# Optimization experiments

Hardware: AMD Instinct MI355X
Metric: run time of the kernel (lower is better)

Reference implementation:

```python
import jax, jax.numpy as jnp
import numpy as np

N, E, HN, K = 4096, 8192, 1024, 8
NF, EF = 128, 64
NH = [256, 256]
EH = [64, 64]
EMB = NH[-1] + len(EH)  # 258
BN_EPS = 1e-5


def setup_inputs() -> dict:
    key = jax.random.key(0)
    ks = jax.random.split(key, 16)

    def nrm(k, shape, fan):
        return jax.random.normal(k, shape, jnp.float32) / np.float32(np.sqrt(fan))

    return {
        "X_n": jax.random.normal(ks[0], (N, NF), jnp.float32),
        "X_e": jax.random.normal(ks[1], (E, EF), jnp.float32),
        # row-normalized-ish adjacency and scaled Laplacian to keep activations bounded
        "A_tilde": jax.random.uniform(ks[2], (N, N), jnp.float32) / np.float32(N),
        "L1_tilde": jax.random.normal(ks[3], (E, E), jnp.float32) / np.float32(np.sqrt(E)),
        "B1": jax.random.normal(ks[4], (N, E), jnp.float32) / np.float32(np.sqrt(E)),
        # GNN params (Linear stores weight as [out, in])
        "gnn_W1": nrm(ks[5], (NH[0], NF), NF), "gnn_b1": jnp.zeros((NH[0],), jnp.float32),
        "gnn_W2": nrm(ks[6], (NH[1], NH[0]), NH[0]), "gnn_b2": jnp.zeros((NH[1],), jnp.float32),
        # HoSC layer 1: in=EF, out=EH[0]
        "hosc_W1": nrm(ks[7], (EH[0], EF), EF), "hosc_b1": jnp.zeros((EH[0],), jnp.float32),
        "bn1_g": jnp.ones((EH[0],), jnp.float32), "bn1_b": jnp.zeros((EH[0],), jnp.float32),
        # HoSC layer 2: in=1 (after channel-max), out=EH[1]
        "hosc_W2": nrm(ks[8], (EH[1], 1), 1), "hosc_b2": jnp.zeros((EH[1],), jnp.float32),
        "bn2_g": jnp.ones((EH[1],), jnp.float32), "bn2_b": jnp.zeros((EH[1],), jnp.float32),
        # heads
        "node_W": nrm(ks[9], (1, EMB), EMB), "node_b": jnp.zeros((1,), jnp.float32),
        "edge_W": nrm(ks[10], (1, len(EH)), len(EH)), "edge_b": jnp.zeros((1,), jnp.float32),
        "hyper_W": nrm(ks[11], (1, EMB), EMB), "hyper_b": jnp.zeros((1,), jnp.float32),
        "hyperedges": jax.random.randint(ks[12], (HN, K), 0, N, jnp.int64),
    }


def _bn(x, g, b):
    # training-mode BatchNorm1d: biased batch statistics over rows
    m = jnp.mean(x, axis=0)
    v = jnp.var(x, axis=0)
    return g * (x - m) / jnp.sqrt(v + BN_EPS) + b


def _hosc_layer(Z, L1, W, bias, g, b):
    Zt = Z @ W.T + bias            # [E, out]
    Zc = L1 @ Zt                   # [E, out]
    Zp = jax.nn.relu(_bn(Zc, g, b))
    return jnp.max(Zp, axis=1, keepdims=True)  # [E, 1]


def reference(X_n, X_e, A_tilde, L1_tilde, B1,
              gnn_W1, gnn_b1, gnn_W2, gnn_b2,
              hosc_W1, hosc_b1, bn1_g, bn1_b,
              hosc_W2, hosc_b2, bn2_g, bn2_b,
              node_W, node_b, edge_W, edge_b, hyper_W, hyper_b,
              hyperedges):
    # --- GNN over nodes ---
    H = jax.nn.relu((A_tilde @ X_n) @ gnn_W1.T + gnn_b1)   # [N, 256]
    H_n = jax.nn.relu((A_tilde @ H) @ gnn_W2.T + gnn_b2)   # [N, 256]

    # --- HoSC over edges ---
    Z1 = _hosc_layer(X_e, L1_tilde, hosc_W1, hosc_b1, bn1_g, bn1_b)  # [E, 1]
    Z2 = _hosc_layer(Z1, L1_tilde, hosc_W2, hosc_b2, bn2_g, bn2_b)   # [E, 1]
    Z_H = jnp.concatenate([Z1, Z2], axis=1)                 # [E, 2]

    # --- fuse edge info into nodes ---
    H_e = B1 @ Z_H                                          # [N, 2]
    Hcat = jnp.concatenate([H_n, H_e], axis=1)              # [N, 258]

    node_prob = jax.nn.sigmoid(Hcat @ node_W.T + node_b).squeeze(-1)  # [N]
    edge_prob = jax.nn.sigmoid(Z_H @ edge_W.T + edge_b).squeeze(-1)   # [E]

    # vectorized hyperedge gather-mean-linear-sigmoid (fixed-size hyperedges)
    hfeat = Hcat[hyperedges].mean(axis=1)                   # [HN, 258]
    hyperedge_prob = jax.nn.sigmoid(hfeat @ hyper_W.T + hyper_b)  # [HN, 1]

    return node_prob, edge_prob, hyperedge_prob, Hcat
```

## Files before the change

kernel.cpp:

```cpp
#include <hip/hip_runtime.h>
#include <hip/hip_bf16.h>

using f32x4  = __attribute__((ext_vector_type(4))) float;
using u32x4  = __attribute__((ext_vector_type(4))) unsigned int;
using bf16x8 = __attribute__((ext_vector_type(8))) short;

__device__ __forceinline__ ushort f2bf(float x) {
    union { __hip_bfloat16 h; ushort u; } cv;
    cv.h = __float2bfloat16(x);
    return cv.u;
}
__device__ __forceinline__ unsigned pk2(float lo, float hi) {
    return (unsigned)f2bf(lo) | ((unsigned)f2bf(hi) << 16);
}
__device__ __forceinline__ float sigmoidf_(float x) { return 1.f / (1.f + expf(-x)); }

template<int NSUM, bool A_BF16, bool ABR, bool SPLIT, bool RELU, bool BF16_OUT, bool HAS_BIAS>
__device__ __forceinline__ void gemm_body(
    ushort* As, ushort* Bs,
    const void* __restrict__ Avoid, const ushort* __restrict__ B,
    const float* __restrict__ abias, const float* __restrict__ bias,
    float* __restrict__ Cf, ushort* __restrict__ Cb,
    int M, int N, int K, int ldc, int kPerChunk, long pStride,
    int bx, int by, int bz)
{
    const int tid  = threadIdx.x;
    const int lane = tid & 63;
    const int wid  = tid >> 6;
    const int wr   = wid >> 1, wc = wid & 1;
    const int g    = lane >> 4, lr = lane & 15;
    const long m0  = (long)bx * 128;
    const int  n0  = by * 64;

    int kbeg = 0, kend = K;
    if (SPLIT) { kbeg = bz * kPerChunk; kend = kbeg + kPerChunk; if (kend > K) kend = K; }

    const int bkr = tid & 31;
    const int bcb = tid >> 5;

    const float*  Af = (const float*)Avoid;
    const ushort* Ab = (const ushort*)Avoid;

    f32x4 pa[4];
    u32x4 pab[2];
    u32x4 pb;

    auto loadT = [&](int k0) {
        if (A_BF16) {
#pragma unroll
            for (int i = 0; i < 2; i++) {
                int s = tid + 256 * i; int row = s >> 2, c8 = s & 3;
                pab[i] = *(const u32x4*)(Ab + (m0 + row) * (long)K + k0 + c8 * 8);
            }
        } else {
#pragma unroll
            for (int i = 0; i < 4; i++) {
                int s = tid + 256 * i; int row = s >> 3, c4 = s & 7;
                const float* base = Af + (m0 + row) * (long)K + k0 + c4 * 4;
                f32x4 v = *(const f32x4*)base;
                if (NSUM > 0) {
#pragma unroll
                    for (int z = 1; z < NSUM; z++) v += *(const f32x4*)(base + z * pStride);
                }
                if (ABR) {
                    f32x4 bq = *(const f32x4*)(abias + k0 + c4 * 4);
                    v.x = fmaxf(v.x + bq.x, 0.f);
                    v.y = fmaxf(v.y + bq.y, 0.f);
                    v.z = fmaxf(v.z + bq.z, 0.f);
                    v.w = fmaxf(v.w + bq.w, 0.f);
                }
                pa[i] = v;
            }
        }
        pb = *(const u32x4*)(B + (long)(k0 + bkr) * N + n0 + bcb * 8);
    };
    auto storeT = [&]() {
        if (A_BF16) {
#pragma unroll
            for (int i = 0; i < 2; i++) {
                int s = tid + 256 * i; int row = s >> 2, c8 = s & 3;
                *(u32x4*)(&As[row * 40 + c8 * 8]) = pab[i];
            }
        } else {
#pragma unroll
            for (int i = 0; i < 4; i++) {
                int s = tid + 256 * i; int row = s >> 3, c4 = s & 7;
                ushort4 w;
                w.x = f2bf(pa[i].x); w.y = f2bf(pa[i].y);
                w.z = f2bf(pa[i].z); w.w = f2bf(pa[i].w);
                *(ushort4*)(&As[row * 40 + c4 * 4]) = w;
            }
        }
        const ushort* p8 = (const ushort*)&pb;
#pragma unroll
        for (int j = 0; j < 8; j++) Bs[(bcb * 8 + j) * 40 + bkr] = p8[j];
    };

    f32x4 acc[4][2] = {};

    const int nk = (kend - kbeg) >> 5;
    loadT(kbeg);
    for (int t = 0; t < nk; ++t) {
        storeT();
        __syncthreads();
        if (t + 1 < nk) loadT(kbeg + ((t + 1) << 5));
        bf16x8 af[4], bfr[2];
#pragma unroll
        for (int fm = 0; fm < 4; fm++)
            af[fm] = *(const bf16x8*)(&As[(wr * 64 + fm * 16 + lr) * 40 + g * 8]);
#pragma unroll
        for (int fn = 0; fn < 2; fn++)
            bfr[fn] = *(const bf16x8*)(&Bs[(wc * 32 + fn * 16 + lr) * 40 + g * 8]);
#pragma unroll
        for (int fm = 0; fm < 4; fm++)
#pragma unroll
            for (int fn = 0; fn < 2; fn++)
                acc[fm][fn] = __builtin_amdgcn_mfma_f32_16x16x32_bf16(af[fm], bfr[fn], acc[fm][fn], 0, 0, 0);
        __syncthreads();
    }

    if (SPLIT) {
        float* P = Cf + (long)bz * M * N;
#pragma unroll
        for (int fm = 0; fm < 4; fm++)
#pragma unroll
            for (int fn = 0; fn < 2; fn++)
#pragma unroll
                for (int rr = 0; rr < 4; rr++) {
                    long row = m0 + wr * 64 + fm * 16 + g * 4 + rr;
                    int  col = n0 + wc * 32 + fn * 16 + lr;
                    P[row * N + col] = acc[fm][fn][rr];
                }
    } else {
#pragma unroll
        for (int fm = 0; fm < 4; fm++)
#pragma unroll
            for (int fn = 0; fn < 2; fn++)
#pragma unroll
                for (int rr = 0; rr < 4; rr++) {
                    long row = m0 + wr * 64 + fm * 16 + g * 4 + rr;
                    int  col = n0 + wc * 32 + fn * 16 + lr;
                    float v = acc[fm][fn][rr];
                    if (HAS_BIAS) v += bias[col];
                    if (RELU) v = fmaxf(v, 0.f);
                    if (BF16_OUT) Cb[row * ldc + col] = f2bf(v);
                    else          Cf[row * ldc + col] = v;
                }
    }
}

__global__ __launch_bounds__(256)
void prep_k(const float* __restrict__ A, ushort* __restrict__ Abf,
            const float* __restrict__ Xn, const float* __restrict__ W1, ushort* __restrict__ T1,
            const float* __restrict__ Xe, const float* __restrict__ Wh,
            const float* __restrict__ hb, ushort* __restrict__ Zt1,
            const float* __restrict__ W2, ushort* __restrict__ W2t,
            float* __restrict__ stats)
{
    __shared__ float xs[1024];
    int b = blockIdx.x, t = threadIdx.x;
    if (b < 8192) {
        long j = (long)b * 256 + t;
        f32x4 v0 = ((const f32x4*)A)[2 * j];
        f32x4 v1 = ((const f32x4*)A)[2 * j + 1];
        u32x4 w;
        w.x = pk2(v0.x, v0.y); w.y = pk2(v0.z, v0.w);
        w.z = pk2(v1.x, v1.y); w.w = pk2(v1.z, v1.w);
        ((u32x4*)Abf)[j] = w;
    } else if (b < 8704) {
        int r0 = (b - 8192) * 8;
        for (int idx = t; idx < 1024; idx += 256) xs[idx] = Xn[(long)r0 * 128 + idx];
        __syncthreads();
        float acc[8] = {};
        const float* wrow = W1 + (long)t * 128;
        for (int i = 0; i < 128; i++) {
            float w = wrow[i];
#pragma unroll
            for (int r = 0; r < 8; r++) acc[r] += xs[r * 128 + i] * w;
        }
#pragma unroll
        for (int r = 0; r < 8; r++) T1[(long)(r0 + r) * 256 + t] = f2bf(acc[r]);
    } else if (b < 10752) {
        int row = (b - 8704) * 4 + (t >> 6);
        int o   = t & 63;
        const float* xr = Xe + (long)row * 64;
        const float* wr = Wh + (long)o * 64;
        float acc = hb[o];
#pragma unroll 8
        for (int i = 0; i < 64; i++) acc += xr[i] * wr[i];
        Zt1[(long)row * 64 + o] = f2bf(acc);
    } else if (b < 11008) {
        int j = (b - 10752) * 256 + t;
        int i = j >> 8, o = j & 255;
        W2t[j] = f2bf(W2[o * 256 + i]);
    } else {
        if (t < 256) stats[t] = 0.f;
    }
}

__device__ __forceinline__ void bnred_body(int b, const float* __restrict__ P,
                                           float* __restrict__ Zc,
                                           float* __restrict__ gsum, float* __restrict__ gsq)
{
    const long MN = 8192 * 64;
    int t = threadIdx.x;
    int c = t & 63, rg = t >> 6;
    float sx = 0.f, sq = 0.f;
    int base = b * 32 + rg;
#pragma unroll 4
    for (int i = 0; i < 8; i++) {
        long idx = (long)(base + 4 * i) * 64 + c;
        float x = 0.f;
#pragma unroll
        for (int z = 0; z < 8; z++) x += P[idx + z * MN];
        Zc[idx] = x;
        sx += x; sq += x * x;
    }
    __shared__ float ls[256], lq[256];
    ls[t] = sx; lq[t] = sq;
    __syncthreads();
    if (t < 64) {
        float a = ls[t] + ls[t + 64] + ls[t + 128] + ls[t + 192];
        float q = lq[t] + lq[t + 64] + lq[t + 128] + lq[t + 192];
        atomicAdd(&gsum[t], a);
        atomicAdd(&gsq[t], q);
    }
}

__device__ __forceinline__ void z1_body(int b, const float* __restrict__ Zc,
                                        const float* __restrict__ gsum, const float* __restrict__ gsq,
                                        const float* __restrict__ g, const float* __restrict__ bb,
                                        float* __restrict__ Z1)
{
    int w = threadIdx.x >> 6, lane = threadIdx.x & 63;
    int row = b * 4 + w;
    const float inv = 1.f / 8192.f;
    float m = gsum[lane] * inv;
    float v = gsq[lane] * inv - m * m;
    float x = Zc[row * 64 + lane];
    float y = fmaxf(g[lane] * (x - m) * rsqrtf(v + 1e-5f) + bb[lane], 0.f);
#pragma unroll
    for (int o = 32; o > 0; o >>= 1) y = fmaxf(y, __shfl_xor(y, o));
    if (lane == 0) Z1[row] = y;
}

__device__ __forceinline__ void pass2_body(int row, const float* __restrict__ L1,
                                           const float* __restrict__ Z1,
                                           float* __restrict__ s, float* __restrict__ r)
{
    int t = threadIdx.x;
    int l = t & 63, w = t >> 6;
    const f32x4* rp = (const f32x4*)(L1 + (long)row * 8192);
    const f32x4* z4 = (const f32x4*)Z1;
    float as = 0.f, ar = 0.f;
#pragma unroll 4
    for (int k = 0; k < 8; k++) {
        f32x4 v = rp[t + 256 * k];
        f32x4 z = z4[t + 256 * k];
        as += v.x * z.x + v.y * z.y + v.z * z.z + v.w * z.w;
        ar += v.x + v.y + v.z + v.w;
    }
#pragma unroll
    for (int o = 32; o > 0; o >>= 1) { as += __shfl_xor(as, o); ar += __shfl_xor(ar, o); }
    __shared__ float sw[4], rw[4];
    if (l == 0) { sw[w] = as; rw[w] = ar; }
    __syncthreads();
    if (t == 0) {
        s[row] = sw[0] + sw[1] + sw[2] + sw[3];
        r[row] = rw[0] + rw[1] + rw[2] + rw[3];
    }
    __syncthreads();
}

__device__ __forceinline__ void hcatred_body(int b, const float* __restrict__ P,
                                             const float* __restrict__ b2, float* __restrict__ hcat)
{
    const long MNq = (long)4096 * 256 / 4;
    int j = b * 256 + threadIdx.x;
    int row = j >> 6, c4 = (j & 63) * 4;
    const f32x4* Q = (const f32x4*)P;
    f32x4 v = Q[j] + Q[j + MNq] + Q[j + 2 * MNq] + Q[j + 3 * MNq];
    f32x4 bq = *(const f32x4*)(b2 + c4);
    float* dst = hcat + (long)row * 258 + c4;
    float2 lo = { fmaxf(v.x + bq.x, 0.f), fmaxf(v.y + bq.y, 0.f) };
    float2 hi = { fmaxf(v.z + bq.z, 0.f), fmaxf(v.w + bq.w, 0.f) };
    *(float2*)dst = lo;
    *(float2*)(dst + 2) = hi;
}

__global__ __launch_bounds__(256)
void dual_a_k(const float* __restrict__ L1, const ushort* __restrict__ Zt1, float* __restrict__ Pa,
              const ushort* __restrict__ Abf, const ushort* __restrict__ T1, float* __restrict__ Pb)
{
    __shared__ ushort As[128 * 40];
    __shared__ ushort Bs[64 * 40];
    int bid = blockIdx.x;
    if (bid < 512) {
        gemm_body<0, false, false, true, false, false, false>(
            As, Bs, L1, Zt1, nullptr, nullptr, Pa, nullptr,
            8192, 64, 8192, 64, 1024, 0, bid & 63, 0, bid >> 6);
    } else {
        int b = bid - 512;
        gemm_body<0, true, false, true, false, false, false>(
            As, Bs, Abf, T1, nullptr, nullptr, Pb, nullptr,
            4096, 256, 4096, 256, 1024, 0, b & 31, (b >> 5) & 3, b >> 7);
    }
}

__global__ __launch_bounds__(256)
void dual_b_k(const float* __restrict__ Pb, const float* __restrict__ gb1,
              const ushort* __restrict__ W2t, ushort* __restrict__ T2,
              const float* __restrict__ Pa, float* __restrict__ Zc1,
              float* __restrict__ gsum, float* __restrict__ gsq)
{
    __shared__ ushort As[128 * 40];
    __shared__ ushort Bs[64 * 40];
    int bid = blockIdx.x;
    if (bid < 128) {
        gemm_body<4, false, true, false, false, true, false>(
            As, Bs, Pb, W2t, gb1, nullptr, nullptr, T2,
            4096, 256, 256, 256, 0, (long)4096 * 256, bid & 31, bid >> 5, 0);
    } else {
        bnred_body(bid - 128, Pa, Zc1, gsum, gsq);
    }
}

__global__ __launch_bounds__(256)
void dual_c_k(const ushort* __restrict__ Abf, const ushort* __restrict__ T2, float* __restrict__ Pa,
              const float* __restrict__ Zc1, const float* __restrict__ gsum,
              const float* __restrict__ gsq, const float* __restrict__ bn1g,
              const float* __restrict__ bn1b, float* __restrict__ Z1)
{
    __shared__ ushort As[128 * 40];
    __shared__ ushort Bs[64 * 40];
    int bid = blockIdx.x;
    if (bid < 512) {
        gemm_body<0, true, false, true, false, false, false>(
            As, Bs, Abf, T2, nullptr, nullptr, Pa, nullptr,
            4096, 256, 4096, 256, 1024, 0, bid & 31, (bid >> 5) & 3, bid >> 7);
    } else {
        z1_body(bid - 512, Zc1, gsum, gsq, bn1g, bn1b, Z1);
    }
}

__global__ __launch_bounds__(256)
void dual_d_k(const float* __restrict__ Pa, const float* __restrict__ gb2, float* __restrict__ hcat,
              const float* __restrict__ L1, const float* __restrict__ Z1,
              float* __restrict__ s, float* __restrict__ r)
{
    int bid = blockIdx.x;
    if (bid < 1024) {
        hcatred_body(bid, Pa, gb2, hcat);
    } else {
        int pb = bid - 1024;
#pragma unroll
        for (int i = 0; i < 4; i++)
            pass2_body(i * 2048 + pb, L1, Z1, s, r);
    }
}

__global__ __launch_bounds__(256)
void z2_edge_k(const float* __restrict__ s, const float* __restrict__ r,
               const float* __restrict__ W2, const float* __restrict__ b2,
               const float* __restrict__ g2, const float* __restrict__ bb2,
               const float* __restrict__ eW, const float* __restrict__ eb,
               const float* __restrict__ Z1,
               float* __restrict__ Z2, float* __restrict__ edge_out)
{
    int t = threadIdx.x, l = t & 63, w = t >> 6;
    float Ss = 0, Sr = 0, Sss = 0, Srr = 0, Ssr = 0;
    for (int i = t; i < 8192; i += 256) {
        float sv = s[i], rv = r[i];
        Ss += sv; Sr += rv; Sss += sv * sv; Srr += rv * rv; Ssr += sv * rv;
    }
#pragma unroll
    for (int o = 32; o > 0; o >>= 1) {
        Ss += __shfl_xor(Ss, o); Sr += __shfl_xor(Sr, o);
        Sss += __shfl_xor(Sss, o); Srr += __shfl_xor(Srr, o); Ssr += __shfl_xor(Ssr, o);
    }
    __shared__ float buf[4][5];
    if (l == 0) { buf[w][0] = Ss; buf[w][1] = Sr; buf[w][2] = Sss; buf[w][3] = Srr; buf[w][4] = Ssr; }
    __syncthreads();
    float S0 = buf[0][0] + buf[1][0] + buf[2][0] + buf[3][0];
    float S1 = buf[0][1] + buf[1][1] + buf[2][1] + buf[3][1];
    float S2 = buf[0][2] + buf[1][2] + buf[2][2] + buf[3][2];
    float S3 = buf[0][3] + buf[1][3] + buf[2][3] + buf[3][3];
    float S4 = buf[0][4] + buf[1][4] + buf[2][4] + buf[3][4];

    int row = blockIdx.x * 4 + w;
    const float inv = 1.f / 8192.f;
    float ms = S0 * inv, mr = S1 * inv;
    float vs = S2 * inv - ms * ms;
    float vr = S3 * inv - mr * mr;
    float cv = S4 * inv - ms * mr;
    float w2 = W2[l], bz = b2[l];
    float mc = w2 * ms + bz * mr;
    float vc = w2 * w2 * vs + 2.f * w2 * bz * cv + bz * bz * vr;
    float x  = w2 * s[row] + bz * r[row];
    float y  = fmaxf(g2[l] * (x - mc) * rsqrtf(vc + 1e-5f) + bb2[l], 0.f);
#pragma unroll
    for (int o = 32; o > 0; o >>= 1) y = fmaxf(y, __shfl_xor(y, o));
    if (l == 0) {
        Z2[row] = y;
        float e = Z1[row] * eW[0] + y * eW[1] + eb[0];
        edge_out[row] = sigmoidf_(e);
    }
}

__global__ __launch_bounds__(256) void he_node_k(const float* __restrict__ B1, const float* __restrict__ Z1,
                                                 const float* __restrict__ Z2, float* __restrict__ hcat,
                                                 const float* __restrict__ nW, const float* __restrict__ nb,
                                                 float* __restrict__ node_out)
{
    int t = threadIdx.x;
    int l = t & 63, w = t >> 6;
    __shared__ float s1[4], s2[4], s3[4];
    const f32x4* z1v = (const f32x4*)Z1;
    const f32x4* z2v = (const f32x4*)Z2;
#pragma unroll
    for (int i = 0; i < 4; i++) {
        int n = i * 1024 + blockIdx.x;
        const f32x4* rp = (const f32x4*)(B1 + (long)n * 8192);
        float a1 = 0.f, a2 = 0.f;
#pragma unroll 4
        for (int k = 0; k < 8; k++) {
            f32x4 v = rp[t + 256 * k];
            f32x4 p = z1v[t + 256 * k];
            f32x4 q = z2v[t + 256 * k];
            a1 += v.x * p.x + v.y * p.y + v.z * p.z + v.w * p.w;
            a2 += v.x * q.x + v.y * q.y + v.z * q.z + v.w * q.w;
        }
        float d = hcat[(long)n * 258 + t] * nW[t];
#pragma unroll
        for (int o = 32; o > 0; o >>= 1) {
            a1 += __shfl_xor(a1, o); a2 += __shfl_xor(a2, o); d += __shfl_xor(d, o);
        }
        if (l == 0) { s1[w] = a1; s2[w] = a2; s3[w] = d; }
        __syncthreads();
        if (t == 0) {
            float A1 = s1[0] + s1[1] + s1[2] + s1[3];
            float A2 = s2[0] + s2[1] + s2[2] + s2[3];
            float D  = s3[0] + s3[1] + s3[2] + s3[3];
            hcat[(long)n * 258 + 256] = A1;
            hcat[(long)n * 258 + 257] = A2;
            node_out[n] = sigmoidf_(D + A1 * nW[256] + A2 * nW[257] + nb[0]);
        }
        __syncthreads();
    }
}

__global__ __launch_bounds__(256) void hyper_k(const void* __restrict__ he_idx,
                                               const float* __restrict__ hcat,
                                               const float* __restrict__ hW, const float* __restrict__ hb,
                                               float* __restrict__ out)
{
    int w = threadIdx.x >> 6, lane = threadIdx.x & 63;
    int h = blockIdx.x * 4 + w;
    const unsigned int* u = (const unsigned int*)he_idx;
    unsigned int odd = u[2 * lane + 1];
    bool is64 = __all(odd == 0u);
    float acc = 0.f;
    for (int k = 0; k < 8; k++) {
        int idx;
        if (is64) idx = (int)((const long long*)he_idx)[h * 8 + k];
        else      idx = ((const int*)he_idx)[h * 8 + k];
        const float* hr = hcat + (long)idx * 258;
        for (int d = lane; d < 258; d += 64) acc += hr[d] * hW[d];
    }
    acc *= 0.125f;
#pragma unroll
    for (int o = 32; o > 0; o >>= 1) acc += __shfl_xor(acc, o);
    if (lane == 0) out[h] = sigmoidf_(acc + hb[0]);
}

extern "C" void kernel_launch(void* const* d_in, const int* in_sizes, int n_in,
                              void* d_out, int out_size, void* d_ws, size_t ws_size,
                              hipStream_t stream)
{
    const float* X_n  = (const float*)d_in[0];
    const float* X_e  = (const float*)d_in[1];
    const float* A_t  = (const float*)d_in[2];
    const float* L1   = (const float*)d_in[3];
    const float* B1   = (const float*)d_in[4];
    const float* gW1  = (const float*)d_in[5];
    const float* gb1  = (const float*)d_in[6];
    const float* gW2  = (const float*)d_in[7];
    const float* gb2  = (const float*)d_in[8];
    const float* hW1  = (const float*)d_in[9];
    const float* hb1  = (const float*)d_in[10];
    const float* bn1g = (const float*)d_in[11];
    const float* bn1b = (const float*)d_in[12];
    const float* hW2  = (const float*)d_in[13];
    const float* hb2  = (const float*)d_in[14];
    const float* bn2g = (const float*)d_in[15];
    const float* bn2b = (const float*)d_in[16];
    const float* nW   = (const float*)d_in[17];
    const float* nb   = (const float*)d_in[18];
    const float* eW   = (const float*)d_in[19];
    const float* ebb  = (const float*)d_in[20];
    const float* yW   = (const float*)d_in[21];
    const float* yb   = (const float*)d_in[22];
    const void*  he   = d_in[23];

    float* out       = (float*)d_out;
    float* out_node  = out;
    float* out_edge  = out + 4096;
    float* out_hyper = out + 12288;
    float* hcat      = out + 13312;

    size_t off = 0;
    auto alloc = [&](size_t bytes) {
        void* p = (char*)d_ws + off;
        off = (off + bytes + 255) & ~(size_t)255;
        return p;
    };
    ushort* Abf    = (ushort*)alloc((size_t)4096 * 4096 * 2);
    ushort* T1     = (ushort*)alloc(4096 * 256 * 2);
    ushort* T2     = (ushort*)alloc(4096 * 256 * 2);
    ushort* Zt1    = (ushort*)alloc(8192 * 64 * 2);
    ushort* W2t    = (ushort*)alloc(256 * 256 * 2);
    float*  Zc1    = (float*)alloc(8192 * 64 * 4);
    float*  stats  = (float*)alloc(256 * 4);
    float*  gsum   = stats;
    float*  gsq    = stats + 64;
    float*  Z1     = (float*)alloc(8192 * 4);
    float*  Z2     = (float*)alloc(8192 * 4);
    float*  sbuf   = (float*)alloc(8192 * 4);
    float*  rbuf   = (float*)alloc(8192 * 4);
    float*  Pa     = (float*)alloc((size_t)8192 * 64 * 8 * 4);
    float*  Pb     = (float*)alloc((size_t)4096 * 256 * 4 * 4);

    prep_k<<<11009, 256, 0, stream>>>(A_t, Abf, X_n, gW1, T1, X_e, hW1, hb1, Zt1,
                                      gW2, W2t, stats);

    dual_a_k<<<1024, 256, 0, stream>>>(L1, Zt1, Pa, Abf, T1, Pb);

    dual_b_k<<<384, 256, 0, stream>>>(Pb, gb1, W2t, T2, Pa, Zc1, gsum, gsq);

    dual_c_k<<<2560, 256, 0, stream>>>(Abf, T2, Pa, Zc1, gsum, gsq, bn1g, bn1b, Z1);

    dual_d_k<<<3072, 256, 0, stream>>>(Pa, gb2, hcat, L1, Z1, sbuf, rbuf);

    z2_edge_k<<<2048, 256, 0, stream>>>(sbuf, rbuf, hW2, hb2, bn2g, bn2b,
                                        eW, ebb, Z1, Z2, out_edge);

    he_node_k<<<1024, 256, 0, stream>>>(B1, Z1, Z2, hcat, nW, nb, out_node);

    hyper_k<<<256, 256, 0, stream>>>(he, hcat, yW, yb, out_hyper);
}
```

Baseline: 301.7 us.

## Merge all stage kernels into one persistent cooperative kernel with grid syncs

Replaces the eight separate kernel launches with one cooperative persistent kernel. Each former kernel becomes a grid-stride phase separated by __threadfence and grid.sync, and the grid is sized from the occupancy query (capped at 2048 blocks). The aim is to remove per-launch overhead and inter-kernel gaps. In exchange, the phases are limited to a fixed resident grid, grid-wide barriers are added, and the launch-bounds occupancy hint may constrain registers in the GEMM phases.

```diff
diff --git a/kernel.cpp b/kernel.cpp
--- a/kernel.cpp
+++ b/kernel.cpp
@@ -1,5 +1,8 @@
 #include <hip/hip_runtime.h>
 #include <hip/hip_bf16.h>
+#include <hip/hip_cooperative_groups.h>
+
+namespace cg = cooperative_groups;
 
 using f32x4  = __attribute__((ext_vector_type(4))) float;
 using u32x4  = __attribute__((ext_vector_type(4))) unsigned int;
@@ -149,278 +152,235 @@
     }
 }
 
-__global__ __launch_bounds__(256)
-void prep_k(const float* __restrict__ A, ushort* __restrict__ Abf,
-            const float* __restrict__ Xn, const float* __restrict__ W1, ushort* __restrict__ T1,
-            const float* __restrict__ Xe, const float* __restrict__ Wh,
-            const float* __restrict__ hb, ushort* __restrict__ Zt1,
-            const float* __restrict__ W2, ushort* __restrict__ W2t,
-            float* __restrict__ stats)
+struct MegaArgs {
+    const float *A, *Xn, *W1, *Xe, *Wh, *hb1, *W2;
+    ushort *Abf, *T1, *Zt1, *W2t, *T2;
+    const float *L1, *B1;
+    float *stats;
+    float *Zc1, *Z1, *Z2, *sbuf, *rbuf, *Pa, *Pb;
+    const float *gb1, *gb2, *bn1g, *bn1b, *hW2, *hb2, *bn2g, *bn2b;
+    const float *nW, *nb, *eW, *eb, *yW, *yb;
+    const void  *he;
+    float *hcat, *out_node, *out_edge, *out_hyper;
+};
+
+__global__ __launch_bounds__(256, 4) void mega_k(MegaArgs a)
 {
-    __shared__ float xs[1024];
-    int b = blockIdx.x, t = threadIdx.x;
-    if (b < 8192) {
-        long j = (long)b * 256 + t;
-        f32x4 v0 = ((const f32x4*)A)[2 * j];
-        f32x4 v1 = ((const f32x4*)A)[2 * j + 1];
-        u32x4 w;
-        w.x = pk2(v0.x, v0.y); w.y = pk2(v0.z, v0.w);
-        w.z = pk2(v1.x, v1.y); w.w = pk2(v1.z, v1.w);
-        ((u32x4*)Abf)[j] = w;
-    } else if (b < 8704) {
-        int r0 = (b - 8192) * 8;
-        for (int idx = t; idx < 1024; idx += 256) xs[idx] = Xn[(long)r0 * 128 + idx];
-        __syncthreads();
-        float acc[8] = {};
-        const float* wrow = W1 + (long)t * 128;
-        for (int i = 0; i < 128; i++) {
-            float w = wrow[i];
-#pragma unroll
-            for (int r = 0; r < 8; r++) acc[r] += xs[r * 128 + i] * w;
-        }
-#pragma unroll
-        for (int r = 0; r < 8; r++) T1[(long)(r0 + r) * 256 + t] = f2bf(acc[r]);
-    } else if (b < 10752) {
-        int row = (b - 8704) * 4 + (t >> 6);
-        int o   = t & 63;
-        const float* xr = Xe + (long)row * 64;
-        const float* wr = Wh + (long)o * 64;
-        float acc = hb[o];
-#pragma unroll 8
-        for (int i = 0; i < 64; i++) acc += xr[i] * wr[i];
-        Zt1[(long)row * 64 + o] = f2bf(acc);
-    } else if (b < 11008) {
-        int j = (b - 10752) * 256 + t;
-        int i = j >> 8, o = j & 255;
-        W2t[j] = f2bf(W2[o * 256 + i]);
-    } else {
-        if (t < 256) stats[t] = 0.f;
-    }
-}
-
-__device__ __forceinline__ void bnred_body(int b, const float* __restrict__ P,
-                                           float* __restrict__ Zc,
-                                           float* __restrict__ gsum, float* __restrict__ gsq)
-{
-    const long MN = 8192 * 64;
-    int t = threadIdx.x;
-    int c = t & 63, rg = t >> 6;
-    float sx = 0.f, sq = 0.f;
-    int base = b * 32 + rg;
-#pragma unroll 4
-    for (int i = 0; i < 8; i++) {
-        long idx = (long)(base + 4 * i) * 64 + c;
-        float x = 0.f;
-#pragma unroll
-        for (int z = 0; z < 8; z++) x += P[idx + z * MN];
-        Zc[idx] = x;
-        sx += x; sq += x * x;
-    }
-    __shared__ float ls[256], lq[256];
-    ls[t] = sx; lq[t] = sq;
-    __syncthreads();
-    if (t < 64) {
-        float a = ls[t] + ls[t + 64] + ls[t + 128] + ls[t + 192];
-        float q = lq[t] + lq[t + 64] + lq[t + 128] + lq[t + 192];
-        atomicAdd(&gsum[t], a);
-        atomicAdd(&gsq[t], q);
-    }
-}
-
-__device__ __forceinline__ void z1_body(int b, const float* __restrict__ Zc,
-                                        const float* __restrict__ gsum, const float* __restrict__ gsq,
-                                        const float* __restrict__ g, const float* __restrict__ bb,
-                                        float* __restrict__ Z1)
-{
-    int w = threadIdx.x >> 6, lane = threadIdx.x & 63;
-    int row = b * 4 + w;
-    const float inv = 1.f / 8192.f;
-    float m = gsum[lane] * inv;
-    float v = gsq[lane] * inv - m * m;
-    float x = Zc[row * 64 + lane];
-    float y = fmaxf(g[lane] * (x - m) * rsqrtf(v + 1e-5f) + bb[lane], 0.f);
-#pragma unroll
-    for (int o = 32; o > 0; o >>= 1) y = fmaxf(y, __shfl_xor(y, o));
-    if (lane == 0) Z1[row] = y;
-}
-
-__device__ __forceinline__ void pass2_body(int row, const float* __restrict__ L1,
-                                           const float* __restrict__ Z1,
-                                           float* __restrict__ s, float* __restrict__ r)
-{
-    int t = threadIdx.x;
-    int l = t & 63, w = t >> 6;
-    const f32x4* rp = (const f32x4*)(L1 + (long)row * 8192);
-    const f32x4* z4 = (const f32x4*)Z1;
-    float as = 0.f, ar = 0.f;
-#pragma unroll 4
-    for (int k = 0; k < 8; k++) {
-        f32x4 v = rp[t + 256 * k];
-        f32x4 z = z4[t + 256 * k];
-        as += v.x * z.x + v.y * z.y + v.z * z.z + v.w * z.w;
-        ar += v.x + v.y + v.z + v.w;
-    }
-#pragma unroll
-    for (int o = 32; o > 0; o >>= 1) { as += __shfl_xor(as, o); ar += __shfl_xor(ar, o); }
-    __shared__ float sw[4], rw[4];
-    if (l == 0) { sw[w] = as; rw[w] = ar; }
-    __syncthreads();
-    if (t == 0) {
-        s[row] = sw[0] + sw[1] + sw[2] + sw[3];
-        r[row] = rw[0] + rw[1] + rw[2] + rw[3];
-    }
-    __syncthreads();
-}
-
-__device__ __forceinline__ void hcatred_body(int b, const float* __restrict__ P,
-                                             const float* __restrict__ b2, float* __restrict__ hcat)
-{
-    const long MNq = (long)4096 * 256 / 4;
-    int j = b * 256 + threadIdx.x;
-    int row = j >> 6, c4 = (j & 63) * 4;
-    const f32x4* Q = (const f32x4*)P;
-    f32x4 v = Q[j] + Q[j + MNq] + Q[j + 2 * MNq] + Q[j + 3 * MNq];
-    f32x4 bq = *(const f32x4*)(b2 + c4);
-    float* dst = hcat + (long)row * 258 + c4;
-    float2 lo = { fmaxf(v.x + bq.x, 0.f), fmaxf(v.y + bq.y, 0.f) };
-    float2 hi = { fmaxf(v.z + bq.z, 0.f), fmaxf(v.w + bq.w, 0.f) };
-    *(float2*)dst = lo;
-    *(float2*)(dst + 2) = hi;
-}
-
-__global__ __launch_bounds__(256)
-void dual_a_k(const float* __restrict__ L1, const ushort* __restrict__ Zt1, float* __restrict__ Pa,
-              const ushort* __restrict__ Abf, const ushort* __restrict__ T1, float* __restrict__ Pb)
-{
+    cg::grid_group grid = cg::this_grid();
     __shared__ ushort As[128 * 40];
     __shared__ ushort Bs[64 * 40];
-    int bid = blockIdx.x;
-    if (bid < 512) {
-        gemm_body<0, false, false, true, false, false, false>(
-            As, Bs, L1, Zt1, nullptr, nullptr, Pa, nullptr,
-            8192, 64, 8192, 64, 1024, 0, bid & 63, 0, bid >> 6);
-    } else {
-        int b = bid - 512;
-        gemm_body<0, true, false, true, false, false, false>(
-            As, Bs, Abf, T1, nullptr, nullptr, Pb, nullptr,
-            4096, 256, 4096, 256, 1024, 0, b & 31, (b >> 5) & 3, b >> 7);
-    }
-}
-
-__global__ __launch_bounds__(256)
-void dual_b_k(const float* __restrict__ Pb, const float* __restrict__ gb1,
-              const ushort* __restrict__ W2t, ushort* __restrict__ T2,
-              const float* __restrict__ Pa, float* __restrict__ Zc1,
-              float* __restrict__ gsum, float* __restrict__ gsq)
-{
-    __shared__ ushort As[128 * 40];
-    __shared__ ushort Bs[64 * 40];
-    int bid = blockIdx.x;
-    if (bid < 128) {
-        gemm_body<4, false, true, false, false, true, false>(
-            As, Bs, Pb, W2t, gb1, nullptr, nullptr, T2,
-            4096, 256, 256, 256, 0, (long)4096 * 256, bid & 31, bid >> 5, 0);
-    } else {
-        bnred_body(bid - 128, Pa, Zc1, gsum, gsq);
-    }
-}
-
-__global__ __launch_bounds__(256)
-void dual_c_k(const ushort* __restrict__ Abf, const ushort* __restrict__ T2, float* __restrict__ Pa,
-              const float* __restrict__ Zc1, const float* __restrict__ gsum,
-              const float* __restrict__ gsq, const float* __restrict__ bn1g,
-              const float* __restrict__ bn1b, float* __restrict__ Z1)
-{
-    __shared__ ushort As[128 * 40];
-    __shared__ ushort Bs[64 * 40];
-    int bid = blockIdx.x;
-    if (bid < 512) {
-        gemm_body<0, true, false, true, false, false, false>(
-            As, Bs, Abf, T2, nullptr, nullptr, Pa, nullptr,
-            4096, 256, 4096, 256, 1024, 0, bid & 31, (bid >> 5) & 3, bid >> 7);
-    } else {
-        z1_body(bid - 512, Zc1, gsum, gsq, bn1g, bn1b, Z1);
-    }
-}
-
-__global__ __launch_bounds__(256)
-void dual_d_k(const float* __restrict__ Pa, const float* __restrict__ gb2, float* __restrict__ hcat,
-              const float* __restrict__ L1, const float* __restrict__ Z1,
-              float* __restrict__ s, float* __restrict__ r)
-{
-    int bid = blockIdx.x;
-    if (bid < 1024) {
-        hcatred_body(bid, Pa, gb2, hcat);
-    } else {
-        int pb = bid - 1024;
-#pragma unroll
-        for (int i = 0; i < 4; i++)
-            pass2_body(i * 2048 + pb, L1, Z1, s, r);
-    }
-}
-
-__global__ __launch_bounds__(256)
-void z2_edge_k(const float* __restrict__ s, const float* __restrict__ r,
-               const float* __restrict__ W2, const float* __restrict__ b2,
-               const float* __restrict__ g2, const float* __restrict__ bb2,
-               const float* __restrict__ eW, const float* __restrict__ eb,
-               const float* __restrict__ Z1,
-               float* __restrict__ Z2, float* __restrict__ edge_out)
-{
-    int t = threadIdx.x, l = t & 63, w = t >> 6;
-    float Ss = 0, Sr = 0, Sss = 0, Srr = 0, Ssr = 0;
-    for (int i = t; i < 8192; i += 256) {
-        float sv = s[i], rv = r[i];
-        Ss += sv; Sr += rv; Sss += sv * sv; Srr += rv * rv; Ssr += sv * rv;
-    }
-#pragma unroll
-    for (int o = 32; o > 0; o >>= 1) {
-        Ss += __shfl_xor(Ss, o); Sr += __shfl_xor(Sr, o);
-        Sss += __shfl_xor(Sss, o); Srr += __shfl_xor(Srr, o); Ssr += __shfl_xor(Ssr, o);
-    }
-    __shared__ float buf[4][5];
-    if (l == 0) { buf[w][0] = Ss; buf[w][1] = Sr; buf[w][2] = Sss; buf[w][3] = Srr; buf[w][4] = Ssr; }
-    __syncthreads();
-    float S0 = buf[0][0] + buf[1][0] + buf[2][0] + buf[3][0];
-    float S1 = buf[0][1] + buf[1][1] + buf[2][1] + buf[3][1];
-    float S2 = buf[0][2] + buf[1][2] + buf[2][2] + buf[3][2];
-    float S3 = buf[0][3] + buf[1][3] + buf[2][3] + buf[3][3];
-    float S4 = buf[0][4] + buf[1][4] + buf[2][4] + buf[3][4];
-
-    int row = blockIdx.x * 4 + w;
-    const float inv = 1.f / 8192.f;
-    float ms = S0 * inv, mr = S1 * inv;
-    float vs = S2 * inv - ms * ms;
-    float vr = S3 * inv - mr * mr;
-    float cv = S4 * inv - ms * mr;
-    float w2 = W2[l], bz = b2[l];
-    float mc = w2 * ms + bz * mr;
-    float vc = w2 * w2 * vs + 2.f * w2 * bz * cv + bz * bz * vr;
-    float x  = w2 * s[row] + bz * r[row];
-    float y  = fmaxf(g2[l] * (x - mc) * rsqrtf(vc + 1e-5f) + bb2[l], 0.f);
-#pragma unroll
-    for (int o = 32; o > 0; o >>= 1) y = fmaxf(y, __shfl_xor(y, o));
-    if (l == 0) {
-        Z2[row] = y;
-        float e = Z1[row] * eW[0] + y * eW[1] + eb[0];
-        edge_out[row] = sigmoidf_(e);
-    }
-}
-
-__global__ __launch_bounds__(256) void he_node_k(const float* __restrict__ B1, const float* __restrict__ Z1,
-                                                 const float* __restrict__ Z2, float* __restrict__ hcat,
-                                                 const float* __restrict__ nW, const float* __restrict__ nb,
-                                                 float* __restrict__ node_out)
-{
-    int t = threadIdx.x;
-    int l = t & 63, w = t >> 6;
-    __shared__ float s1[4], s2[4], s3[4];
-    const f32x4* z1v = (const f32x4*)Z1;
-    const f32x4* z2v = (const f32x4*)Z2;
-#pragma unroll
-    for (int i = 0; i < 4; i++) {
-        int n = i * 1024 + blockIdx.x;
-        const f32x4* rp = (const f32x4*)(B1 + (long)n * 8192);
+    const int G = gridDim.x;
+    const int t = threadIdx.x;
+    const int l = t & 63, w = t >> 6;
+
+    for (int u = blockIdx.x; u < 11009; u += G) {
+        if (u < 8192) {
+            long j = (long)u * 256 + t;
+            f32x4 v0 = ((const f32x4*)a.A)[2 * j];
+            f32x4 v1 = ((const f32x4*)a.A)[2 * j + 1];
+            u32x4 wv;
+            wv.x = pk2(v0.x, v0.y); wv.y = pk2(v0.z, v0.w);
+            wv.z = pk2(v1.x, v1.y); wv.w = pk2(v1.z, v1.w);
+            ((u32x4*)a.Abf)[j] = wv;
+        } else if (u < 8704) {
+            float* xs = (float*)As;
+            int r0 = (u - 8192) * 8;
+            __syncthreads();
+            for (int idx = t; idx < 1024; idx += 256) xs[idx] = a.Xn[(long)r0 * 128 + idx];
+            __syncthreads();
+            float acc[8] = {};
+            const float* wrow = a.W1 + (long)t * 128;
+            for (int i = 0; i < 128; i++) {
+                float wv = wrow[i];
+#pragma unroll
+                for (int r = 0; r < 8; r++) acc[r] += xs[r * 128 + i] * wv;
+            }
+#pragma unroll
+            for (int r = 0; r < 8; r++) a.T1[(long)(r0 + r) * 256 + t] = f2bf(acc[r]);
+        } else if (u < 10752) {
+            int row = (u - 8704) * 4 + w;
+            int o   = l;
+            const float* xr = a.Xe + (long)row * 64;
+            const float* wr = a.Wh + (long)o * 64;
+            float acc = a.hb1[o];
+#pragma unroll 8
+            for (int i = 0; i < 64; i++) acc += xr[i] * wr[i];
+            a.Zt1[(long)row * 64 + o] = f2bf(acc);
+        } else if (u < 11008) {
+            int j = (u - 10752) * 256 + t;
+            int i = j >> 8, o = j & 255;
+            a.W2t[j] = f2bf(a.W2[o * 256 + i]);
+        } else {
+            if (t < 128) a.stats[t] = 0.f;
+        }
+    }
+    __threadfence();
+    grid.sync();
+
+    for (int u = blockIdx.x; u < 1024; u += G) {
+        if (u < 512) {
+            gemm_body<0, false, false, true, false, false, false>(
+                As, Bs, a.L1, a.Zt1, nullptr, nullptr, a.Pa, nullptr,
+                8192, 64, 8192, 64, 1024, 0, u & 63, 0, u >> 6);
+        } else {
+            int b = u - 512;
+            gemm_body<0, true, false, true, false, false, false>(
+                As, Bs, a.Abf, a.T1, nullptr, nullptr, a.Pb, nullptr,
+                4096, 256, 4096, 256, 1024, 0, b & 31, (b >> 5) & 3, b >> 7);
+        }
+    }
+    __threadfence();
+    grid.sync();
+
+    for (int u = blockIdx.x; u < 384; u += G) {
+        if (u < 128) {
+            gemm_body<4, false, true, false, false, true, false>(
+                As, Bs, a.Pb, a.W2t, a.gb1, nullptr, nullptr, a.T2,
+                4096, 256, 256, 256, 0, (long)4096 * 256, u & 31, u >> 5, 0);
+        } else {
+            int b = u - 128;
+            const long MN = 8192 * 64;
+            int c = t & 63, rg = t >> 6;
+            float sx = 0.f, sq = 0.f;
+            int base = b * 32 + rg;
+#pragma unroll 4
+            for (int i = 0; i < 8; i++) {
+                long idx = (long)(base + 4 * i) * 64 + c;
+                float x = 0.f;
+#pragma unroll
+                for (int z = 0; z < 8; z++) x += a.Pa[idx + z * MN];
+                a.Zc1[idx] = x;
+                sx += x; sq += x * x;
+            }
+            float* ls = (float*)Bs;
+            float* lq = ls + 256;
+            __syncthreads();
+            ls[t] = sx; lq[t] = sq;
+            __syncthreads();
+            if (t < 64) {
+                float av = ls[t] + ls[t + 64] + ls[t + 128] + ls[t + 192];
+                float qv = lq[t] + lq[t + 64] + lq[t + 128] + lq[t + 192];
+                atomicAdd(&a.stats[t], av);
+                atomicAdd(&a.stats[64 + t], qv);
+            }
+            __syncthreads();
+        }
+    }
+    __threadfence();
+    grid.sync();
+
+    for (int u = blockIdx.x; u < 2560; u += G) {
+        if (u < 512) {
+            gemm_body<0, true, false, true, false, false, false>(
+                As, Bs, a.Abf, a.T2, nullptr, nullptr, a.Pa, nullptr,
+                4096, 256, 4096, 256, 1024, 0, u & 31, (u >> 5) & 3, u >> 7);
+        } else {
+            int b = u - 512;
+            int row = b * 4 + w;
+            const float inv = 1.f / 8192.f;
+            float m = a.stats[l] * inv;
+            float v = a.stats[64 + l] * inv - m * m;
+            float x = a.Zc1[row * 64 + l];
+            float y = fmaxf(a.bn1g[l] * (x - m) * rsqrtf(v + 1e-5f) + a.bn1b[l], 0.f);
+#pragma unroll
+            for (int o = 32; o > 0; o >>= 1) y = fmaxf(y, __shfl_xor(y, o));
+            if (l == 0) a.Z1[row] = y;
+        }
+    }
+    __threadfence();
+    grid.sync();
+
+    for (int u = blockIdx.x; u < 9216; u += G) {
+        if (u < 1024) {
+            const long MNq = (long)4096 * 256 / 4;
+            int j = u * 256 + t;
+            int row = j >> 6, c4 = (j & 63) * 4;
+            const f32x4* Q = (const f32x4*)a.Pa;
+            f32x4 v = Q[j] + Q[j + MNq] + Q[j + 2 * MNq] + Q[j + 3 * MNq];
+            f32x4 bq = *(const f32x4*)(a.gb2 + c4);
+            float* dst = a.hcat + (long)row * 258 + c4;
+            float2 lo = { fmaxf(v.x + bq.x, 0.f), fmaxf(v.y + bq.y, 0.f) };
+            float2 hi = { fmaxf(v.z + bq.z, 0.f), fmaxf(v.w + bq.w, 0.f) };
+            *(float2*)dst = lo;
+            *(float2*)(dst + 2) = hi;
+        } else {
+            int row = u - 1024;
+            const f32x4* rp = (const f32x4*)(a.L1 + (long)row * 8192);
+            const f32x4* z4 = (const f32x4*)a.Z1;
+            float as = 0.f, ar = 0.f;
+#pragma unroll 4
+            for (int k = 0; k < 8; k++) {
+                f32x4 v = rp[t + 256 * k];
+                f32x4 z = z4[t + 256 * k];
+                as += v.x * z.x + v.y * z.y + v.z * z.z + v.w * z.w;
+                ar += v.x + v.y + v.z + v.w;
+            }
+#pragma unroll
+            for (int o = 32; o > 0; o >>= 1) { as += __shfl_xor(as, o); ar += __shfl_xor(ar, o); }
+            float* sw = (float*)Bs;
+            float* rw = sw + 4;
+            __syncthreads();
+            if (l == 0) { sw[w] = as; rw[w] = ar; }
+            __syncthreads();
+            if (t == 0) {
+                a.sbuf[row] = sw[0] + sw[1] + sw[2] + sw[3];
+                a.rbuf[row] = rw[0] + rw[1] + rw[2] + rw[3];
+            }
+            __syncthreads();
+        }
+    }
+    __threadfence();
+    grid.sync();
+
+    for (int u = blockIdx.x; u < 2048; u += G) {
+        float Ss = 0, Sr = 0, Sss = 0, Srr = 0, Ssr = 0;
+        for (int i = t; i < 8192; i += 256) {
+            float sv = a.sbuf[i], rv = a.rbuf[i];
+            Ss += sv; Sr += rv; Sss += sv * sv; Srr += rv * rv; Ssr += sv * rv;
+        }
+#pragma unroll
+        for (int o = 32; o > 0; o >>= 1) {
+            Ss += __shfl_xor(Ss, o); Sr += __shfl_xor(Sr, o);
+            Sss += __shfl_xor(Sss, o); Srr += __shfl_xor(Srr, o); Ssr += __shfl_xor(Ssr, o);
+        }
+        float* buf = (float*)Bs;
+        __syncthreads();
+        if (l == 0) { buf[w * 5 + 0] = Ss; buf[w * 5 + 1] = Sr; buf[w * 5 + 2] = Sss; buf[w * 5 + 3] = Srr; buf[w * 5 + 4] = Ssr; }
+        __syncthreads();
+        float S0 = buf[0] + buf[5] + buf[10] + buf[15];
+        float S1 = buf[1] + buf[6] + buf[11] + buf[16];
+        float S2 = buf[2] + buf[7] + buf[12] + buf[17];
+        float S3 = buf[3] + buf[8] + buf[13] + buf[18];
+        float S4 = buf[4] + buf[9] + buf[14] + buf[19];
+        __syncthreads();
+
+        int row = u * 4 + w;
+        const float inv = 1.f / 8192.f;
+        float ms = S0 * inv, mr = S1 * inv;
+        float vs = S2 * inv - ms * ms;
+        float vr = S3 * inv - mr * mr;
+        float cv = S4 * inv - ms * mr;
+        float w2 = a.hW2[l], bz = a.hb2[l];
+        float mc = w2 * ms + bz * mr;
+        float vc = w2 * w2 * vs + 2.f * w2 * bz * cv + bz * bz * vr;
+        float x  = w2 * a.sbuf[row] + bz * a.rbuf[row];
+        float y  = fmaxf(a.bn2g[l] * (x - mc) * rsqrtf(vc + 1e-5f) + a.bn2b[l], 0.f);
+#pragma unroll
+        for (int o = 32; o > 0; o >>= 1) y = fmaxf(y, __shfl_xor(y, o));
+        if (l == 0) {
+            a.Z2[row] = y;
+            float e = a.Z1[row] * a.eW[0] + y * a.eW[1] + a.eb[0];
+            a.out_edge[row] = sigmoidf_(e);
+        }
+    }
+    __threadfence();
+    grid.sync();
+
+    for (int u = blockIdx.x; u < 4096; u += G) {
+        int n = u;
+        const f32x4* rp  = (const f32x4*)(a.B1 + (long)n * 8192);
+        const f32x4* z1v = (const f32x4*)a.Z1;
+        const f32x4* z2v = (const f32x4*)a.Z2;
         float a1 = 0.f, a2 = 0.f;
 #pragma unroll 4
         for (int k = 0; k < 8; k++) {
@@ -430,47 +390,48 @@
             a1 += v.x * p.x + v.y * p.y + v.z * p.z + v.w * p.w;
             a2 += v.x * q.x + v.y * q.y + v.z * q.z + v.w * q.w;
         }
-        float d = hcat[(long)n * 258 + t] * nW[t];
+        float d = a.hcat[(long)n * 258 + t] * a.nW[t];
 #pragma unroll
         for (int o = 32; o > 0; o >>= 1) {
             a1 += __shfl_xor(a1, o); a2 += __shfl_xor(a2, o); d += __shfl_xor(d, o);
         }
+        float* s1 = (float*)Bs;
+        float* s2 = s1 + 4;
+        float* s3 = s2 + 4;
+        __syncthreads();
         if (l == 0) { s1[w] = a1; s2[w] = a2; s3[w] = d; }
         __syncthreads();
         if (t == 0) {
             float A1 = s1[0] + s1[1] + s1[2] + s1[3];
             float A2 = s2[0] + s2[1] + s2[2] + s2[3];
             float D  = s3[0] + s3[1] + s3[2] + s3[3];
-            hcat[(long)n * 258 + 256] = A1;
-            hcat[(long)n * 258 + 257] = A2;
-            node_out[n] = sigmoidf_(D + A1 * nW[256] + A2 * nW[257] + nb[0]);
-        }
-        __syncthreads();
-    }
-}
-
-__global__ __launch_bounds__(256) void hyper_k(const void* __restrict__ he_idx,
-                                               const float* __restrict__ hcat,
-                                               const float* __restrict__ hW, const float* __restrict__ hb,
-                                               float* __restrict__ out)
-{
-    int w = threadIdx.x >> 6, lane = threadIdx.x & 63;
-    int h = blockIdx.x * 4 + w;
-    const unsigned int* u = (const unsigned int*)he_idx;
-    unsigned int odd = u[2 * lane + 1];
-    bool is64 = __all(odd == 0u);
-    float acc = 0.f;
-    for (int k = 0; k < 8; k++) {
-        int idx;
-        if (is64) idx = (int)((const long long*)he_idx)[h * 8 + k];
-        else      idx = ((const int*)he_idx)[h * 8 + k];
-        const float* hr = hcat + (long)idx * 258;
-        for (int d = lane; d < 258; d += 64) acc += hr[d] * hW[d];
-    }
-    acc *= 0.125f;
-#pragma unroll
-    for (int o = 32; o > 0; o >>= 1) acc += __shfl_xor(acc, o);
-    if (lane == 0) out[h] = sigmoidf_(acc + hb[0]);
+            a.hcat[(long)n * 258 + 256] = A1;
+            a.hcat[(long)n * 258 + 257] = A2;
+            a.out_node[n] = sigmoidf_(D + A1 * a.nW[256] + A2 * a.nW[257] + a.nb[0]);
+        }
+        __syncthreads();
+    }
+    __threadfence();
+    grid.sync();
+
+    for (int u = blockIdx.x; u < 256; u += G) {
+        int h = u * 4 + w;
+        const unsigned int* uu = (const unsigned int*)a.he;
+        unsigned int odd = uu[2 * l + 1];
+        bool is64 = __all(odd == 0u);
+        float acc = 0.f;
+        for (int k = 0; k < 8; k++) {
+            int idx;
+            if (is64) idx = (int)((const long long*)a.he)[h * 8 + k];
+            else      idx = ((const int*)a.he)[h * 8 + k];
+            const float* hr = a.hcat + (long)idx * 258;
+            for (int d = l; d < 258; d += 64) acc += hr[d] * a.yW[d];
+        }
+        acc *= 0.125f;
+#pragma unroll
+        for (int o = 32; o > 0; o >>= 1) acc += __shfl_xor(acc, o);
+        if (l == 0) a.out_hyper[h] = sigmoidf_(acc + a.yb[0]);
+    }
 }
 
 extern "C" void kernel_launch(void* const* d_in, const int* in_sizes, int n_in,
@@ -521,8 +482,6 @@
     ushort* W2t    = (ushort*)alloc(256 * 256 * 2);
     float*  Zc1    = (float*)alloc(8192 * 64 * 4);
     float*  stats  = (float*)alloc(256 * 4);
-    float*  gsum   = stats;
-    float*  gsq    = stats + 64;
     float*  Z1     = (float*)alloc(8192 * 4);
     float*  Z2     = (float*)alloc(8192 * 4);
     float*  sbuf   = (float*)alloc(8192 * 4);
@@ -530,21 +489,25 @@
     float*  Pa     = (float*)alloc((size_t)8192 * 64 * 8 * 4);
     float*  Pb     = (float*)alloc((size_t)4096 * 256 * 4 * 4);
 
-    prep_k<<<11009, 256, 0, stream>>>(A_t, Abf, X_n, gW1, T1, X_e, hW1, hb1, Zt1,
-                                      gW2, W2t, stats);
-
-    dual_a_k<<<1024, 256, 0, stream>>>(L1, Zt1, Pa, Abf, T1, Pb);
-
-    dual_b_k<<<384, 256, 0, stream>>>(Pb, gb1, W2t, T2, Pa, Zc1, gsum, gsq);
-
-    dual_c_k<<<2560, 256, 0, stream>>>(Abf, T2, Pa, Zc1, gsum, gsq, bn1g, bn1b, Z1);
-
-    dual_d_k<<<3072, 256, 0, stream>>>(Pa, gb2, hcat, L1, Z1, sbuf, rbuf);
-
-    z2_edge_k<<<2048, 256, 0, stream>>>(sbuf, rbuf, hW2, hb2, bn2g, bn2b,
-                                        eW, ebb, Z1, Z2, out_edge);
-
-    he_node_k<<<1024, 256, 0, stream>>>(B1, Z1, Z2, hcat, nW, nb, out_node);
-
-    hyper_k<<<256, 256, 0, stream>>>(he, hcat, yW, yb, out_hyper);
+    MegaArgs a;
+    a.A = A_t; a.Xn = X_n; a.W1 = gW1; a.Xe = X_e; a.Wh = hW1; a.hb1 = hb1; a.W2 = gW2;
+    a.Abf = Abf; a.T1 = T1; a.Zt1 = Zt1; a.W2t = W2t; a.T2 = T2;
+    a.L1 = L1; a.B1 = B1;
+    a.stats = stats;
+    a.Zc1 = Zc1; a.Z1 = Z1; a.Z2 = Z2; a.sbuf = sbuf; a.rbuf = rbuf; a.Pa = Pa; a.Pb = Pb;
+    a.gb1 = gb1; a.gb2 = gb2; a.bn1g = bn1g; a.bn1b = bn1b;
+    a.hW2 = hW2; a.hb2 = hb2; a.bn2g = bn2g; a.bn2b = bn2b;
+    a.nW = nW; a.nb = nb; a.eW = eW; a.eb = ebb; a.yW = yW; a.yb = yb;
+    a.he = he;
+    a.hcat = hcat; a.out_node = out_node; a.out_edge = out_edge; a.out_hyper = out_hyper;
+
+    int maxB = 0;
+    hipOccupancyMaxActiveBlocksPerMultiprocessor(&maxB, (const void*)mega_k, 256, 0);
+    if (maxB < 1) maxB = 1;
+    long grid = (long)maxB * 256;
+    if (grid > 2048) grid = 2048;
+
+    void* params[] = { &a };
+    hipLaunchCooperativeKernel((const void*)mega_k, dim3((unsigned)grid), dim3(256),
+                               params, 0, stream);
 }
```

Result: slower. 1.057 ms (+250.4%).
